# Performance work log

Hardware: AMD Instinct MI355X
Metric: run time of the kernel (lower is better)

Reference implementation:

```python
import jax, jax.numpy as jnp
import numpy as np

EMBED_DIM = 1024
Q_DIM = 512
KV_DIM = 512
NUM_HEADS = 16
HEAD_DIM = EMBED_DIM // NUM_HEADS
EPS = 1e-5


def setup_inputs() -> dict:
    key = jax.random.key(0)
    ks = jax.random.split(key, 13)
    B, N1, N2 = 2, 2048, 2048
    s_q = 1.0 / np.sqrt(Q_DIM)
    s_kv = 1.0 / np.sqrt(KV_DIM)
    s_e = 1.0 / np.sqrt(EMBED_DIM)
    return {
        "query": jax.random.normal(ks[0], (B, N1, Q_DIM), jnp.float32),
        "key": jax.random.normal(ks[1], (B, N2, KV_DIM), jnp.float32),
        "value": jax.random.normal(ks[2], (B, N2, KV_DIM), jnp.float32),
        "Wq": jax.random.uniform(ks[3], (Q_DIM, EMBED_DIM), jnp.float32, -s_q, s_q),
        "bq": jax.random.uniform(ks[4], (EMBED_DIM,), jnp.float32, -s_q, s_q),
        "Wk": jax.random.uniform(ks[5], (KV_DIM, EMBED_DIM), jnp.float32, -s_kv, s_kv),
        "bk": jax.random.uniform(ks[6], (EMBED_DIM,), jnp.float32, -s_kv, s_kv),
        "Wv": jax.random.uniform(ks[7], (KV_DIM, EMBED_DIM), jnp.float32, -s_kv, s_kv),
        "bv": jax.random.uniform(ks[8], (EMBED_DIM,), jnp.float32, -s_kv, s_kv),
        "Wo": jax.random.uniform(ks[9], (EMBED_DIM, EMBED_DIM), jnp.float32, -s_e, s_e),
        "bo": jax.random.uniform(ks[10], (EMBED_DIM,), jnp.float32, -s_e, s_e),
        "gamma": jnp.ones((EMBED_DIM,), jnp.float32),
        "beta": jnp.zeros((EMBED_DIM,), jnp.float32),
    }


def reference(query, key, value, Wq, bq, Wk, bk, Wv, bv, Wo, bo, gamma, beta):
    B, N1, _ = query.shape
    _, N2, _ = key.shape
    scale = HEAD_DIM ** (-0.5)
    # projections -> [B, H, N, D]
    Q = (query @ Wq + bq).reshape(B, N1, NUM_HEADS, HEAD_DIM).transpose(0, 2, 1, 3)
    K = (key @ Wk + bk).reshape(B, N2, NUM_HEADS, HEAD_DIM).transpose(0, 2, 1, 3)
    V = (value @ Wv + bv).reshape(B, N2, NUM_HEADS, HEAD_DIM).transpose(0, 2, 1, 3)
    # full score matrix [B, H, N1, N2] (matches original eager attention)
    att = jnp.einsum("bhqd,bhkd->bhqk", Q, K) * scale
    att = jax.nn.softmax(att, axis=-1)
    # dropout is identity in eval mode
    out = jnp.einsum("bhqk,bhkd->bhqd", att, V)  # [B, H, N1, D]
    out = out.transpose(0, 2, 1, 3).reshape(B, N1, EMBED_DIM)
    out = out @ Wo + bo
    # LayerNorm
    mu = out.mean(-1, keepdims=True)
    var = ((out - mu) ** 2).mean(-1, keepdims=True)
    return (out - mu) * jax.lax.rsqrt(var + EPS) * gamma + beta
```

## Files before the change

kernel.cpp:

```cpp
#include <hip/hip_runtime.h>

typedef __bf16 bf16x8 __attribute__((ext_vector_type(8)));
typedef __bf16 bf16x4 __attribute__((ext_vector_type(4)));
typedef float f32x4 __attribute__((ext_vector_type(4)));
typedef unsigned short u16;
typedef unsigned int u32;

__device__ __forceinline__ f32x4 mfma16(bf16x8 a, bf16x8 b, f32x4 c) {
  return __builtin_amdgcn_mfma_f32_16x16x32_bf16(a, b, c, 0, 0, 0);
}

__device__ __forceinline__ void gload_lds16(const void* g, void* l) {
  __builtin_amdgcn_global_load_lds(
      (const __attribute__((address_space(1))) void*)g,
      (__attribute__((address_space(3))) void*)l, 16, 0, 0);
}

__global__ __launch_bounds__(256) void tobf16_3(const float4* __restrict__ a,
                                                const float4* __restrict__ b,
                                                const float4* __restrict__ c,
                                                bf16x4* __restrict__ oa,
                                                bf16x4* __restrict__ ob,
                                                bf16x4* __restrict__ oc, int n4) {
  int i = blockIdx.x * 256 + threadIdx.x;
  if (i >= n4) return;
  const int z = blockIdx.y;
  const float4* in = z == 0 ? a : z == 1 ? b : c;
  bf16x4* out = z == 0 ? oa : z == 1 ? ob : oc;
  float4 v = in[i];
  bf16x4 o;
  o[0] = (__bf16)v.x; o[1] = (__bf16)v.y; o[2] = (__bf16)v.z; o[3] = (__bf16)v.w;
  out[i] = o;
}

__global__ __launch_bounds__(256) void wtrans4(const float* __restrict__ W0,
                                               const float* __restrict__ W1,
                                               const float* __restrict__ W2,
                                               const float* __restrict__ W3,
                                               u16* __restrict__ T0, u16* __restrict__ T1,
                                               u16* __restrict__ T2, u16* __restrict__ T3) {
  const int z = blockIdx.z;
  const int K = (z == 3) ? 1024 : 512;
  const int N = 1024;
  const int k0 = blockIdx.y * 32;
  if (k0 >= K) return;
  const float* W = z == 0 ? W0 : z == 1 ? W1 : z == 2 ? W2 : W3;
  u16* Wt = z == 0 ? T0 : z == 1 ? T1 : z == 2 ? T2 : T3;
  __shared__ float t[32][33];
  const int tx = threadIdx.x, ty = threadIdx.y;
  const int n0 = blockIdx.x * 32;
#pragma unroll
  for (int i = 0; i < 4; ++i)
    t[ty + i * 8][tx] = W[(size_t)(k0 + ty + i * 8) * N + n0 + tx];
  __syncthreads();
#pragma unroll
  for (int i = 0; i < 4; ++i)
    ((__bf16*)Wt)[(size_t)(n0 + ty + i * 8) * K + k0 + tx] = (__bf16)t[tx][ty + i * 8];
}

__global__ __launch_bounds__(256) void vtrans(const u16* __restrict__ Vb,
                                              u16* __restrict__ Vt, int N2) {
  __shared__ __align__(16) u16 t[64][72];
  const int tid = threadIdx.x;
  const int kv0 = blockIdx.x * 64, h = blockIdx.y, b = blockIdx.z;
  const u16* src = Vb + ((size_t)(b * N2 + kv0)) * 1024 + h * 64;
#pragma unroll
  for (int i = 0; i < 2; ++i) {
    int f = i * 256 + tid;
    int r = f >> 3, c = f & 7;
    *(bf16x8*)&t[r][c * 8] = *(const bf16x8*)&src[(size_t)r * 1024 + c * 8];
  }
  __syncthreads();
  u16* dst = Vt + ((size_t)((b * 16 + h) * 64)) * N2 + kv0;
#pragma unroll
  for (int i = 0; i < 2; ++i) {
    int g = i * 256 + tid;
    int d = g >> 3, kc = g & 7;
    union { u16 u[8]; bf16x8 v; } pk;
#pragma unroll
    for (int j = 0; j < 8; ++j) pk.u[j] = t[kc * 8 + j][d];
    *(bf16x8*)&dst[(size_t)d * N2 + kc * 8] = pk.v;
  }
}

template <int OUT_F32, int DBUF>
__device__ __forceinline__ void gemm_body(const u16* __restrict__ A,
                                          const u16* __restrict__ Bt,
                                          const float* __restrict__ bias,
                                          void* __restrict__ Cout,
                                          int M, int N, int K, float scl) {
  constexpr int NB = DBUF ? 2 : 1;
  __shared__ __align__(16) u16 lA[NB][128 * 64];
  __shared__ __align__(16) u16 lB[NB][128 * 64];
  const int tid = threadIdx.x;
  const int w = tid >> 6, l = tid & 63;
  const int li = l & 15, lg = l >> 4;
  const int wm = w & 1, wn = w >> 1;
  const int bm = blockIdx.x * 128, bn = blockIdx.y * 128;

  f32x4 acc[4][4] = {};
  const int nk = K >> 6;

  auto stage = [&](int kt, int bufi) {
    const int k0 = kt << 6;
#pragma unroll
    for (int i = 0; i < 4; ++i) {
      const int c0 = (i * 4 + w) * 64;
      const int f = c0 + l;
      const int r = f >> 3, cs = (f & 7) ^ (r & 7);
      gload_lds16(A + (size_t)(bm + r) * K + k0 + cs * 8, &lA[bufi][c0 * 8]);
      gload_lds16(Bt + (size_t)(bn + r) * K + k0 + cs * 8, &lB[bufi][c0 * 8]);
    }
  };

  int cur = 0;
  if (DBUF) {
    stage(0, 0);
    __syncthreads();
  }

  for (int kt = 0; kt < nk; ++kt) {
    if (DBUF) {
      if (kt + 1 < nk) stage(kt + 1, cur ^ 1);
    } else {
      stage(kt, 0);
      __syncthreads();
    }
    bf16x8 af[4][2], bfr[4][2];
#pragma unroll
    for (int m = 0; m < 4; ++m) {
      const int row = wm * 64 + m * 16 + li;
#pragma unroll
      for (int kk = 0; kk < 2; ++kk) {
        const int kc = (lg + kk * 4) ^ (row & 7);
        af[m][kk] = *(const bf16x8*)&lA[cur][row * 64 + kc * 8];
      }
    }
#pragma unroll
    for (int n = 0; n < 4; ++n) {
      const int row = wn * 64 + n * 16 + li;
#pragma unroll
      for (int kk = 0; kk < 2; ++kk) {
        const int kc = (lg + kk * 4) ^ (row & 7);
        bfr[n][kk] = *(const bf16x8*)&lB[cur][row * 64 + kc * 8];
      }
    }
#pragma unroll
    for (int m = 0; m < 4; ++m)
#pragma unroll
      for (int n = 0; n < 4; ++n) {
        acc[m][n] = mfma16(af[m][0], bfr[n][0], acc[m][n]);
        acc[m][n] = mfma16(af[m][1], bfr[n][1], acc[m][n]);
      }
    __syncthreads();
    if (DBUF) cur ^= 1;
  }

#pragma unroll
  for (int m = 0; m < 4; ++m) {
    const int row0 = bm + wm * 64 + m * 16 + lg * 4;
#pragma unroll
    for (int n = 0; n < 4; ++n) {
      const int col = bn + wn * 64 + n * 16 + li;
      const float bv = bias[col];
#pragma unroll
      for (int r = 0; r < 4; ++r) {
        float v = (acc[m][n][r] + bv) * scl;
        if (OUT_F32)
          ((float*)Cout)[(size_t)(row0 + r) * N + col] = v;
        else
          ((__bf16*)Cout)[(size_t)(row0 + r) * N + col] = (__bf16)v;
      }
    }
  }
}

__global__ __launch_bounds__(256) void gemm_qkv(const u16* __restrict__ xq,
                                                const u16* __restrict__ xk,
                                                const u16* __restrict__ xv,
                                                const u16* __restrict__ wqt,
                                                const u16* __restrict__ wkt,
                                                const u16* __restrict__ wvt,
                                                const float* __restrict__ bq,
                                                const float* __restrict__ bk,
                                                const float* __restrict__ bv,
                                                u16* __restrict__ Qb, u16* __restrict__ Kb,
                                                u16* __restrict__ Vb, float qscale) {
  const int z = blockIdx.z;
  const u16* A = z == 0 ? xq : z == 1 ? xk : xv;
  const u16* Bt = z == 0 ? wqt : z == 1 ? wkt : wvt;
  const float* bias = z == 0 ? bq : z == 1 ? bk : bv;
  u16* C = z == 0 ? Qb : z == 1 ? Kb : Vb;
  gemm_body<0, 0>(A, Bt, bias, C, 4096, 1024, 512, z == 0 ? qscale : 1.0f);
}

__global__ __launch_bounds__(256) void gemm_o(const u16* __restrict__ A,
                                              const u16* __restrict__ Bt,
                                              const float* __restrict__ bias,
                                              u16* __restrict__ C) {
  gemm_body<0, 1>(A, Bt, bias, C, 4096, 1024, 1024, 1.0f);
}

__global__ __launch_bounds__(512) void attn64(const u16* __restrict__ Qb,
                                              const u16* __restrict__ Kb,
                                              const u16* __restrict__ Vt,
                                              u16* __restrict__ Ob,
                                              int N1, int N2) {
  const int tid = threadIdx.x;
  const int w = tid >> 6, l = tid & 63;
  const int li = l & 15, lg = l >> 4;

  const int flat = blockIdx.x + 16 * (blockIdx.y + 16 * blockIdx.z);
  const int xcd = flat & 7, idx = flat >> 3;
  const int qb = idx & 15, pr = idx >> 4;
  const int h = 2 * xcd + (pr & 1);
  const int b = pr >> 1;
  const int q0 = qb * 128;

  __shared__ __align__(16) u16 lK[2][64 * 64];
  __shared__ __align__(16) u16 lV[2][64 * 64];
  __shared__ __align__(16) u32 lP[8][16 * 32];

  const size_t qoff = (size_t)(b * N1 + q0 + w * 16 + li) * 1024 + h * 64;
  const bf16x8 qa0 = *(const bf16x8*)&Qb[qoff + lg * 8];
  const bf16x8 qa1 = *(const bf16x8*)&Qb[qoff + 32 + lg * 8];

  const u16* Kbase = Kb + (size_t)b * N2 * 1024 + h * 64;
  const u16* Vbase = Vt + (size_t)((b * 16 + h) * 64) * N2;

  const int sr = tid >> 3;
  const int sc = (tid & 7) ^ (sr & 7);

  f32x4 o[4] = {};
  float m = -1e30f, lsum = 0.f;
  u32* lPw = &lP[w][0];
  const int sw = (li & 7) << 2;

  const int nt = N2 >> 6;
  int cur = 0;
  gload_lds16(Kbase + (size_t)sr * 1024 + sc * 8, &lK[0][w * 512]);
  gload_lds16(Vbase + (size_t)sr * N2 + sc * 8, &lV[0][w * 512]);
  __syncthreads();

  for (int t = 0; t < nt; ++t) {
    if (t + 1 < nt) {
      gload_lds16(Kbase + (size_t)((t + 1) * 64 + sr) * 1024 + sc * 8, &lK[cur ^ 1][w * 512]);
      gload_lds16(Vbase + (size_t)sr * N2 + (t + 1) * 64 + sc * 8, &lV[cur ^ 1][w * 512]);
    }
    const u16* K_ = lK[cur];
    const u16* V_ = lV[cur];

    f32x4 sv[4];
    __builtin_amdgcn_s_setprio(1);
#pragma unroll
    for (int n = 0; n < 4; ++n) {
      const int row = n * 16 + li;
      const int c0 = lg ^ (li & 7), c1 = (lg + 4) ^ (li & 7);
      bf16x8 k0 = *(const bf16x8*)&K_[row * 64 + c0 * 8];
      bf16x8 k1 = *(const bf16x8*)&K_[row * 64 + c1 * 8];
      f32x4 a = {};
      a = mfma16(k0, qa0, a);
      a = mfma16(k1, qa1, a);
      sv[n] = a;
    }
    __builtin_amdgcn_s_setprio(0);

    f32x4 mx;
#pragma unroll
    for (int r = 0; r < 4; ++r)
      mx[r] = fmaxf(fmaxf(sv[0][r], sv[1][r]), fmaxf(sv[2][r], sv[3][r]));
    float tmax = fmaxf(fmaxf(mx[0], mx[1]), fmaxf(mx[2], mx[3]));
    tmax = fmaxf(tmax, __shfl_xor(tmax, 16, 64));
    tmax = fmaxf(tmax, __shfl_xor(tmax, 32, 64));

    if (!__all(tmax <= m + 8.0f)) {
      const float mn = fmaxf(m, tmax);
      const float alpha = __builtin_amdgcn_exp2f(m - mn);
      m = mn;
      lsum *= alpha;
#pragma unroll
      for (int dt = 0; dt < 4; ++dt) o[dt] *= alpha;
    }

    float s_t = 0.f;
#pragma unroll
    for (int n = 0; n < 4; ++n) {
      float p0 = __builtin_amdgcn_exp2f(sv[n][0] - m);
      float p1 = __builtin_amdgcn_exp2f(sv[n][1] - m);
      float p2 = __builtin_amdgcn_exp2f(sv[n][2] - m);
      float p3 = __builtin_amdgcn_exp2f(sv[n][3] - m);
      s_t += (p0 + p1) + (p2 + p3);
      bf16x4 pk;
      pk[0] = (__bf16)p0; pk[1] = (__bf16)p1; pk[2] = (__bf16)p2; pk[3] = (__bf16)p3;
      *(bf16x4*)&lPw[li * 32 + ((n * 8 + lg * 2) ^ sw)] = pk;
    }
    lsum += s_t;

    __builtin_amdgcn_s_setprio(1);
#pragma unroll
    for (int ks = 0; ks < 2; ++ks) {
      const bf16x8 pf = *(const bf16x8*)&lPw[li * 32 + ((ks * 16 + lg * 4) ^ sw)];
#pragma unroll
      for (int dt = 0; dt < 4; ++dt) {
        const int row = dt * 16 + li;
        const int c = (lg + ks * 4) ^ (li & 7);
        const bf16x8 vf = *(const bf16x8*)&V_[row * 64 + c * 8];
        o[dt] = mfma16(vf, pf, o[dt]);
      }
    }
    __builtin_amdgcn_s_setprio(0);
    __syncthreads();
    cur ^= 1;
  }

  lsum += __shfl_xor(lsum, 16, 64);
  lsum += __shfl_xor(lsum, 32, 64);
  const float inv = 1.f / lsum;

  const size_t orow = (size_t)(b * N1 + q0 + w * 16 + li) * 1024 + h * 64;
#pragma unroll
  for (int dt = 0; dt < 4; ++dt) {
    bf16x4 pk;
#pragma unroll
    for (int r = 0; r < 4; ++r) pk[r] = (__bf16)(o[dt][r] * inv);
    *(bf16x4*)&Ob[orow + dt * 16 + lg * 4] = pk;
  }
}

__global__ __launch_bounds__(256) void lnorm(const u16* __restrict__ X,
                                             const float* __restrict__ gamma,
                                             const float* __restrict__ beta,
                                             float* __restrict__ out) {
  const int row = blockIdx.x;
  const int tid = threadIdx.x;
  const bf16x4 xv = ((const bf16x4*)(X + (size_t)row * 1024))[tid];
  float4 v;
  v.x = (float)xv[0]; v.y = (float)xv[1]; v.z = (float)xv[2]; v.w = (float)xv[3];
  float s = v.x + v.y + v.z + v.w;
  float sq = v.x * v.x + v.y * v.y + v.z * v.z + v.w * v.w;
#pragma unroll
  for (int d = 1; d < 64; d <<= 1) {
    s += __shfl_xor(s, d, 64);
    sq += __shfl_xor(sq, d, 64);
  }
  __shared__ float red[8];
  const int w = tid >> 6, l = tid & 63;
  if (l == 0) { red[w] = s; red[4 + w] = sq; }
  __syncthreads();
  s = red[0] + red[1] + red[2] + red[3];
  sq = red[4] + red[5] + red[6] + red[7];
  const float mu = s * (1.f / 1024.f);
  const float var = sq * (1.f / 1024.f) - mu * mu;
  const float rstd = rsqrtf(var + 1e-5f);
  const float4 g = ((const float4*)gamma)[tid];
  const float4 bb = ((const float4*)beta)[tid];
  float4 o;
  o.x = (v.x - mu) * rstd * g.x + bb.x;
  o.y = (v.y - mu) * rstd * g.y + bb.y;
  o.z = (v.z - mu) * rstd * g.z + bb.z;
  o.w = (v.w - mu) * rstd * g.w + bb.w;
  ((float4*)(out + (size_t)row * 1024))[tid] = o;
}

extern "C" void kernel_launch(void* const* d_in, const int* in_sizes, int n_in,
                              void* d_out, int out_size, void* d_ws, size_t ws_size,
                              hipStream_t stream) {
  const float* query = (const float*)d_in[0];
  const float* key_ = (const float*)d_in[1];
  const float* value = (const float*)d_in[2];
  const float* Wq = (const float*)d_in[3];
  const float* bq = (const float*)d_in[4];
  const float* Wk = (const float*)d_in[5];
  const float* bk = (const float*)d_in[6];
  const float* Wv = (const float*)d_in[7];
  const float* bv = (const float*)d_in[8];
  const float* Wo = (const float*)d_in[9];
  const float* bo = (const float*)d_in[10];
  const float* gamma = (const float*)d_in[11];
  const float* beta = (const float*)d_in[12];

  constexpr int B = 2, N1 = 2048, N2 = 2048, E = 1024, QKD = 512;
  constexpr int M = B * N1;
  const float QSCALE = 0.125f * 1.4426950408889634f;

  char* p = (char*)d_ws;
  auto alloc = [&](size_t bytes) {
    char* r = p;
    p += (bytes + 255) & ~(size_t)255;
    return r;
  };
  u16* xq = (u16*)alloc((size_t)M * QKD * 2);
  u16* xk = (u16*)alloc((size_t)M * QKD * 2);
  u16* xv = (u16*)alloc((size_t)M * QKD * 2);
  u16* wqt = (u16*)alloc((size_t)E * QKD * 2);
  u16* wkt = (u16*)alloc((size_t)E * QKD * 2);
  u16* wvt = (u16*)alloc((size_t)E * QKD * 2);
  u16* wot = (u16*)alloc((size_t)E * E * 2);
  u16* Qb = (u16*)alloc((size_t)M * E * 2);
  u16* Kb = (u16*)alloc((size_t)M * E * 2);
  u16* Vb = (u16*)alloc((size_t)M * E * 2);
  u16* Vt = (u16*)alloc((size_t)M * E * 2);
  u16* ao = (u16*)alloc((size_t)M * E * 2);
  u16* ao2 = (u16*)alloc((size_t)M * E * 2);

  const int n4 = M * QKD / 4;
  tobf16_3<<<dim3((n4 + 255) / 256, 3), 256, 0, stream>>>(
      (const float4*)query, (const float4*)key_, (const float4*)value,
      (bf16x4*)xq, (bf16x4*)xk, (bf16x4*)xv, n4);

  wtrans4<<<dim3(E / 32, 32, 4), dim3(32, 8), 0, stream>>>(
      Wq, Wk, Wv, Wo, wqt, wkt, wvt, wot);

  gemm_qkv<<<dim3(M / 128, E / 128, 3), 256, 0, stream>>>(
      xq, xk, xv, wqt, wkt, wvt, bq, bk, bv, Qb, Kb, Vb, QSCALE);

  vtrans<<<dim3(N2 / 64, 16, B), 256, 0, stream>>>(Vb, Vt, N2);

  attn64<<<dim3(N1 / 128, 16, B), 512, 0, stream>>>(Qb, Kb, Vt, ao, N1, N2);

  gemm_o<<<dim3(M / 128, E / 128), 256, 0, stream>>>(ao, wot, bo, ao2);

  lnorm<<<M, 256, 0, stream>>>(ao2, gamma, beta, (float*)d_out);
}
```

Baseline: 120.2 us.

## Software-pipeline QK^T scores one tile ahead of softmax in attention kernel

```diff
diff --git a/kernel.cpp b/kernel.cpp
--- a/kernel.cpp
+++ b/kernel.cpp
@@ -235,40 +235,49 @@
   float m = -1e30f, lsum = 0.f;
   u32* lPw = &lP[w][0];
   const int sw = (li & 7) << 2;
+  const int ca = lg ^ (li & 7), cb = (lg + 4) ^ (li & 7);
 
   const int nt = N2 >> 6;
-  int cur = 0;
+
   gload_lds16(Kbase + (size_t)sr * 1024 + sc * 8, &lK[0][w * 512]);
+  gload_lds16(Kbase + (size_t)(64 + sr) * 1024 + sc * 8, &lK[1][w * 512]);
   gload_lds16(Vbase + (size_t)sr * N2 + sc * 8, &lV[0][w * 512]);
   __syncthreads();
 
+  f32x4 svA[4], svB[4];
+#pragma unroll
+  for (int n = 0; n < 4; ++n) {
+    const int row = n * 16 + li;
+    bf16x8 k0 = *(const bf16x8*)&lK[0][row * 64 + ca * 8];
+    bf16x8 k1 = *(const bf16x8*)&lK[0][row * 64 + cb * 8];
+    f32x4 a = {};
+    a = mfma16(k0, qa0, a);
+    a = mfma16(k1, qa1, a);
+    svA[n] = a;
+  }
+
   for (int t = 0; t < nt; ++t) {
-    if (t + 1 < nt) {
-      gload_lds16(Kbase + (size_t)((t + 1) * 64 + sr) * 1024 + sc * 8, &lK[cur ^ 1][w * 512]);
-      gload_lds16(Vbase + (size_t)sr * N2 + (t + 1) * 64 + sc * 8, &lV[cur ^ 1][w * 512]);
-    }
-    const u16* K_ = lK[cur];
-    const u16* V_ = lV[cur];
-
-    f32x4 sv[4];
-    __builtin_amdgcn_s_setprio(1);
+    __syncthreads();
+    if (t + 2 < nt)
+      gload_lds16(Kbase + (size_t)((t + 2) * 64 + sr) * 1024 + sc * 8, &lK[t & 1][w * 512]);
+    if (t + 1 < nt)
+      gload_lds16(Vbase + (size_t)sr * N2 + (t + 1) * 64 + sc * 8, &lV[(t + 1) & 1][w * 512]);
+
+    f32x4 mx;
+    const u16* Kn = lK[(t + 1) & 1];
 #pragma unroll
     for (int n = 0; n < 4; ++n) {
-      const int row = n * 16 + li;
-      const int c0 = lg ^ (li & 7), c1 = (lg + 4) ^ (li & 7);
-      bf16x8 k0 = *(const bf16x8*)&K_[row * 64 + c0 * 8];
-      bf16x8 k1 = *(const bf16x8*)&K_[row * 64 + c1 * 8];
-      f32x4 a = {};
-      a = mfma16(k0, qa0, a);
-      a = mfma16(k1, qa1, a);
-      sv[n] = a;
-    }
-    __builtin_amdgcn_s_setprio(0);
-
-    f32x4 mx;
-#pragma unroll
-    for (int r = 0; r < 4; ++r)
-      mx[r] = fmaxf(fmaxf(sv[0][r], sv[1][r]), fmaxf(sv[2][r], sv[3][r]));
+      if (t + 1 < nt) {
+        const int row = n * 16 + li;
+        bf16x8 k0 = *(const bf16x8*)&Kn[row * 64 + ca * 8];
+        bf16x8 k1 = *(const bf16x8*)&Kn[row * 64 + cb * 8];
+        f32x4 a = {};
+        a = mfma16(k0, qa0, a);
+        a = mfma16(k1, qa1, a);
+        svB[n] = a;
+      }
+      mx[n] = fmaxf(fmaxf(svA[n][0], svA[n][1]), fmaxf(svA[n][2], svA[n][3]));
+    }
     float tmax = fmaxf(fmaxf(mx[0], mx[1]), fmaxf(mx[2], mx[3]));
     tmax = fmaxf(tmax, __shfl_xor(tmax, 16, 64));
     tmax = fmaxf(tmax, __shfl_xor(tmax, 32, 64));
@@ -285,10 +294,10 @@
     float s_t = 0.f;
 #pragma unroll
     for (int n = 0; n < 4; ++n) {
-      float p0 = __builtin_amdgcn_exp2f(sv[n][0] - m);
-      float p1 = __builtin_amdgcn_exp2f(sv[n][1] - m);
-      float p2 = __builtin_amdgcn_exp2f(sv[n][2] - m);
-      float p3 = __builtin_amdgcn_exp2f(sv[n][3] - m);
+      float p0 = __builtin_amdgcn_exp2f(svA[n][0] - m);
+      float p1 = __builtin_amdgcn_exp2f(svA[n][1] - m);
+      float p2 = __builtin_amdgcn_exp2f(svA[n][2] - m);
+      float p3 = __builtin_amdgcn_exp2f(svA[n][3] - m);
       s_t += (p0 + p1) + (p2 + p3);
       bf16x4 pk;
       pk[0] = (__bf16)p0; pk[1] = (__bf16)p1; pk[2] = (__bf16)p2; pk[3] = (__bf16)p3;
@@ -296,6 +305,7 @@
     }
     lsum += s_t;
 
+    const u16* V_ = lV[t & 1];
     __builtin_amdgcn_s_setprio(1);
 #pragma unroll
     for (int ks = 0; ks < 2; ++ks) {
@@ -309,8 +319,11 @@
       }
     }
     __builtin_amdgcn_s_setprio(0);
-    __syncthreads();
-    cur ^= 1;
+
+    if (t + 1 < nt) {
+#pragma unroll
+      for (int n = 0; n < 4; ++n) svA[n] = svB[n];
+    }
   }
 
   lsum += __shfl_xor(lsum, 16, 64);
@@ -416,7 +429,7 @@
 
   vtrans<<<dim3(N2 / 64, 16, B), 256, 0, stream>>>(Vb, Vt, N2);
 
-  attn64<<<dim3(N1 / 128, 16, B), 512, 0, stream>>>(Qb, Kb, Vt, ao, N1, N2);
+  attn64<<<dim3(16, 16, B), 512, 0, stream>>>(Qb, Kb, Vt, ao, N1, N2);
 
   gemm_o<<<dim3(M / 128, E / 128), 256, 0, stream>>>(ao, wot, bo, ao2);
 
```

After: 125.9 us. 1.05x slower.
